# Kernel optimization log

Hardware: AMD Instinct MI355X
Metric: run time of the kernel (lower is better)

## Reference

```python
import jax, jax.numpy as jnp
import numpy as np

B, NPROP, NCLS, NPTS, NBQ, NCK = 32, 256, 19, 4096, 64, 64
C, QH, VQ = 256, 768, 8


def setup_inputs() -> dict:
    key = jax.random.key(0)
    ks = jax.random.split(key, 12)
    s = 0.02
    return dict(
        sem_cls_logits=jax.random.normal(ks[0], (B, NPROP, NCLS), jnp.float32),
        prop_features=jax.random.normal(ks[1], (B, NPROP, C), jnp.float32),
        box_corners=jax.random.normal(ks[2], (B, NPROP, 8, 3), jnp.float32),
        enc_xyz=jax.random.uniform(ks[3], (B, NPTS, 3), jnp.float32),
        enc_features=jax.random.normal(ks[4], (B, NPTS, C), jnp.float32),
        pc_min=jnp.zeros((B, 3), jnp.float32),
        pc_max=jnp.ones((B, 3), jnp.float32),
        box_query=jax.random.normal(ks[5], (B, NBQ, 8, 3), jnp.float32),
        box_qmask=jnp.ones((B, NBQ), jnp.float32),
        click_query=jax.random.uniform(ks[6], (B, NCK, 3), jnp.float32),
        click_qmask=jnp.ones((B, NCK), jnp.float32),
        gauss_B=jax.random.normal(ks[7], (3, C // 2), jnp.float32),
        box_w1=jax.random.normal(ks[8], (C, QH), jnp.float32) * s,
        box_b1=jnp.zeros((QH,), jnp.float32),
        box_w2=jax.random.normal(ks[9], (QH, VQ * QH), jnp.float32) * s,
        box_b2=jnp.zeros((VQ * QH,), jnp.float32),
        click_w1=jax.random.normal(ks[10], (2 * C, QH), jnp.float32) * s,
        click_b1=jnp.zeros((QH,), jnp.float32),
        click_w2=jax.random.normal(ks[11], (QH, VQ * QH), jnp.float32) * s,
        click_b2=jnp.zeros((VQ * QH,), jnp.float32),
    )


def _mlp(x, w1, b1, w2, b2):
    h = jax.nn.relu(jnp.einsum('bqc,ch->bqh', x, w1) + b1)
    return jnp.einsum('bqh,ho->bqo', h, w2) + b2


def _forward(sem_cls_logits, prop_features, box_corners, enc_xyz, enc_features,
             pc_min, pc_max, box_query, box_qmask, click_query, click_qmask,
             gauss_B, box_w1, box_b1, box_w2, box_b2,
             click_w1, click_b1, click_w2, click_b2):
    bsz = sem_cls_logits.shape[0]
    # proposal semantic mask: 0 for background (last class)
    prop_sem_mask = (jnp.argmax(sem_cls_logits, -1) != sem_cls_logits.shape[-1] - 1)
    prop_sem_mask = prop_sem_mask.astype(prop_features.dtype)  # [B, nprop]

    # ---- box branch: axis-aligned 3D IoU from box corners, argmax match, gather ----
    mn_p = box_corners.min(-2)  # [B, nprop, 3]
    mx_p = box_corners.max(-2)
    vol_p = jnp.prod(mx_p - mn_p, -1)  # [B, nprop]
    mn_q = box_query.min(-2)   # [B, nq, 3]
    mx_q = box_query.max(-2)
    vol_q = jnp.prod(mx_q - mn_q, -1)  # [B, nq]
    inter = jnp.prod(
        jnp.clip(jnp.minimum(mx_q[:, :, None], mx_p[:, None]) -
                 jnp.maximum(mn_q[:, :, None], mn_p[:, None]), 0.0, None), -1)  # [B,nq,nprop]
    iou = inter / (vol_q[:, :, None] + vol_p[:, None] - inter + 1e-8)
    iou = iou * prop_sem_mask[:, None, :]
    match_idx = jnp.argmax(iou, -1)  # [B, nq]
    box_feat = jnp.take_along_axis(prop_features, match_idx[..., None], axis=1)  # [B,nq,C]
    box_prompt = _mlp(box_feat, box_w1, box_b1, box_w2, box_b2).reshape(bsz, -1, QH)
    box_mask = jnp.repeat(box_qmask[:, :, None], VQ, axis=2).reshape(bsz, -1)

    # ---- click branch: fourier pos emb + nearest-neighbor gather + MLP ----
    xyz01 = (click_query - pc_min[:, None]) / (pc_max - pc_min)[:, None]
    proj = (xyz01 * (2.0 * jnp.pi)) @ gauss_B  # [B, nclick, C//2]
    pos = jnp.concatenate([jnp.sin(proj), jnp.cos(proj)], -1)  # [B, nclick, C]
    # squared distances (argmin equivalent to cdist argmin)
    d2 = jnp.sum((click_query[:, :, None, :] - enc_xyz[:, None, :, :]) ** 2, -1)  # [B,nclick,npts]
    nn_ids = jnp.argmin(d2, -1)  # [B, nclick]
    k_fea = jnp.take_along_axis(enc_features, nn_ids[..., None], axis=1)  # [B,nclick,C]
    click_in = jnp.concatenate([k_fea, pos], -1)  # [B, nclick, 2C]
    click_prompt = _mlp(click_in, click_w1, click_b1, click_w2, click_b2).reshape(bsz, -1, QH)
    click_mask = jnp.repeat(click_qmask[:, :, None], VQ, axis=2).reshape(bsz, -1)

    prompt_feature = jnp.concatenate([box_prompt, click_prompt], axis=1)  # [B,(nq+nclick)*VQ,QH]
    prompt_mask = jnp.concatenate([box_mask, click_mask], axis=1)
    return prompt_feature, prompt_mask


def reference(sem_cls_logits, prop_features, box_corners, enc_xyz, enc_features,
              pc_min, pc_max, box_query, box_qmask, click_query, click_qmask,
              gauss_B, box_w1, box_b1, box_w2, box_b2,
              click_w1, click_b1, click_w2, click_b2):
    return _forward(sem_cls_logits, prop_features, box_corners, enc_xyz, enc_features,
                    pc_min, pc_max, box_query, box_qmask, click_query, click_qmask,
                    gauss_B, box_w1, box_b1, box_w2, box_b2,
                    click_w1, click_b1, click_w2, click_b2)
```

## Files before the change

kernel.cpp:

```cpp
#include <hip/hip_runtime.h>

#define TWO_PI 6.283185307179586f

typedef _Float16 half8 __attribute__((ext_vector_type(8)));
typedef _Float16 half4 __attribute__((ext_vector_type(4)));
typedef float floatx4 __attribute__((ext_vector_type(4)));

__device__ __forceinline__ void async16(const _Float16* g, _Float16* l) {
    __builtin_amdgcn_global_load_lds(
        (const __attribute__((address_space(1))) void*)g,
        (__attribute__((address_space(3))) void*)l, 16, 0, 0);
}

__global__ void prep_prop(const float* __restrict__ logits,
                          const float* __restrict__ corners,
                          float* __restrict__ mn, float* __restrict__ mx,
                          float* __restrict__ vol, float* __restrict__ msk)
{
    int idx = blockIdx.x * 256 + threadIdx.x;
    const float* c = corners + (size_t)idx * 24;
    float mn0 = c[0], mn1 = c[1], mn2 = c[2];
    float mx0 = mn0, mx1 = mn1, mx2 = mn2;
#pragma unroll
    for (int k = 1; k < 8; k++) {
        float v0 = c[k*3+0], v1 = c[k*3+1], v2 = c[k*3+2];
        mn0 = fminf(mn0, v0); mx0 = fmaxf(mx0, v0);
        mn1 = fminf(mn1, v1); mx1 = fmaxf(mx1, v1);
        mn2 = fminf(mn2, v2); mx2 = fmaxf(mx2, v2);
    }
    mn[idx*3+0] = mn0; mn[idx*3+1] = mn1; mn[idx*3+2] = mn2;
    mx[idx*3+0] = mx0; mx[idx*3+1] = mx1; mx[idx*3+2] = mx2;
    vol[idx] = (mx0-mn0)*(mx1-mn1)*(mx2-mn2);
    const float* lg = logits + (size_t)idx * 19;
    float bv = lg[0]; int bi = 0;
#pragma unroll
    for (int k = 1; k < 19; k++) { float v = lg[k]; if (v > bv) { bv = v; bi = k; } }
    msk[idx] = (bi != 18) ? 1.0f : 0.0f;
}

__global__ void box_match(const float* __restrict__ box_query,
                          const float* __restrict__ mn_p, const float* __restrict__ mx_p,
                          const float* __restrict__ vol_p, const float* __restrict__ msk,
                          int* __restrict__ match_idx)
{
    int gq = blockIdx.x * 256 + threadIdx.x;
    int b = gq >> 6;
    const float* cq = box_query + (size_t)gq * 24;
    float mn0 = cq[0], mn1 = cq[1], mn2 = cq[2];
    float mx0 = mn0, mx1 = mn1, mx2 = mn2;
#pragma unroll
    for (int k = 1; k < 8; k++) {
        float v0 = cq[k*3+0], v1 = cq[k*3+1], v2 = cq[k*3+2];
        mn0 = fminf(mn0, v0); mx0 = fmaxf(mx0, v0);
        mn1 = fminf(mn1, v1); mx1 = fmaxf(mx1, v1);
        mn2 = fminf(mn2, v2); mx2 = fmaxf(mx2, v2);
    }
    float volq = (mx0-mn0)*(mx1-mn1)*(mx2-mn2);
    const float* mnb = mn_p + (size_t)b * 768;
    const float* mxb = mx_p + (size_t)b * 768;
    const float* vb  = vol_p + (size_t)b * 256;
    const float* mb  = msk + (size_t)b * 256;
    float best = -1.0f; int bi = 0;
    for (int p = 0; p < 256; p++) {
        float e0 = fminf(mx0, mxb[p*3+0]) - fmaxf(mn0, mnb[p*3+0]); e0 = fmaxf(e0, 0.0f);
        float e1 = fminf(mx1, mxb[p*3+1]) - fmaxf(mn1, mnb[p*3+1]); e1 = fmaxf(e1, 0.0f);
        float e2 = fminf(mx2, mxb[p*3+2]) - fmaxf(mn2, mnb[p*3+2]); e2 = fmaxf(e2, 0.0f);
        float inter = (e0*e1)*e2;
        float iou = inter / (volq + vb[p] - inter + 1e-8f) * mb[p];
        if (iou > best) { best = iou; bi = p; }
    }
    match_idx[gq] = bi;
}

__global__ void click_nn(const float* __restrict__ click_query,
                         const float* __restrict__ enc_xyz,
                         int* __restrict__ nn_ids)
{
    int gq = blockIdx.x * 4 + (threadIdx.x >> 6);
    int lane = threadIdx.x & 63;
    int b = gq >> 6;
    float cx = click_query[gq*3+0];
    float cy = click_query[gq*3+1];
    float cz = click_query[gq*3+2];
    const float* ex = enc_xyz + (size_t)b * 4096 * 3;
    float best = 3.4e38f; int bidx = 0;
    for (int p = lane; p < 4096; p += 64) {
        float dx = cx - ex[p*3+0];
        float dy = cy - ex[p*3+1];
        float dz = cz - ex[p*3+2];
        float d = dx*dx + dy*dy;
        d = d + dz*dz;
        if (d < best) { best = d; bidx = p; }
    }
#pragma unroll
    for (int off = 32; off; off >>= 1) {
        float ov = __shfl_down(best, off);
        int   oi = __shfl_down(bidx, off);
        if (ov < best || (ov == best && oi < bidx)) { best = ov; bidx = oi; }
    }
    if (lane == 0) nn_ids[gq] = bidx;
}

__global__ void gather_pos(const float* __restrict__ prop_features,
                           const float* __restrict__ enc_features,
                           const int* __restrict__ match_idx,
                           const int* __restrict__ nn_ids,
                           const float* __restrict__ cq,
                           const float* __restrict__ pc_min,
                           const float* __restrict__ pc_max,
                           const float* __restrict__ gB,
                           _Float16* __restrict__ box_in,
                           _Float16* __restrict__ click_in)
{
    int row = blockIdx.x;
    int c = threadIdx.x;
    int b = row >> 6;
    box_in[(size_t)row*256 + c] =
        (_Float16)prop_features[((size_t)b*256 + match_idx[row])*256 + c];
    click_in[(size_t)row*512 + c] =
        (_Float16)enc_features[((size_t)b*4096 + nn_ids[row])*256 + c];
    int j = c & 127;
    float m0 = pc_min[b*3+0], m1 = pc_min[b*3+1], m2 = pc_min[b*3+2];
    float tx = (cq[row*3+0] - m0) / (pc_max[b*3+0] - m0) * TWO_PI;
    float ty = (cq[row*3+1] - m1) / (pc_max[b*3+1] - m1) * TWO_PI;
    float tz = (cq[row*3+2] - m2) / (pc_max[b*3+2] - m2) * TWO_PI;
    float p = tx * gB[j] + ty * gB[128+j] + tz * gB[256+j];
    float v = (c < 128) ? sinf(p) : cosf(p);
    click_in[(size_t)row*512 + 256 + c] = (_Float16)v;
}

__device__ __forceinline__ void transpose_core(
    const float* __restrict__ src, _Float16* __restrict__ dst,
    int K, int N, _Float16* t)
{
    int n0 = blockIdx.x * 64, k0 = blockIdx.y * 64;
    int tid = threadIdx.x;
    int r = tid >> 4;
    int c4 = (tid & 15) * 4;
#pragma unroll
    for (int p = 0; p < 4; p++) {
        int k = r + p*16;
        float4 v = *(const float4*)(src + (size_t)(k0+k)*N + n0 + c4);
        t[(c4+0)*68 + k] = (_Float16)v.x;
        t[(c4+1)*68 + k] = (_Float16)v.y;
        t[(c4+2)*68 + k] = (_Float16)v.z;
        t[(c4+3)*68 + k] = (_Float16)v.w;
    }
    __syncthreads();
    int ck = (tid & 15) * 4;
#pragma unroll
    for (int p = 0; p < 4; p++) {
        int n = r + p*16;
        half4 v = *(const half4*)(t + n*68 + ck);
        *(half4*)(dst + (size_t)(n0+n)*K + k0 + ck) = v;
    }
}

__global__ void transpose_w2(const float* __restrict__ s0, const float* __restrict__ s1,
                             _Float16* __restrict__ d0, _Float16* __restrict__ d1)
{
    __shared__ _Float16 t[64*68];
    if (blockIdx.z == 0) transpose_core(s0, d0, 768, 6144, t);
    else                 transpose_core(s1, d1, 768, 6144, t);
}

__global__ void transpose_w1(const float* __restrict__ s0, const float* __restrict__ s1,
                             _Float16* __restrict__ d0, _Float16* __restrict__ d1)
{
    __shared__ _Float16 t[64*68];
    if (blockIdx.z == 0) {
        if (blockIdx.y * 64 >= 256) return;
        transpose_core(s0, d0, 256, 768, t);
    } else {
        transpose_core(s1, d1, 512, 768, t);
    }
}

template<int MODE>
__device__ __forceinline__ void gemm_core(
    const _Float16* __restrict__ A, const _Float16* __restrict__ Bt,
    const float* __restrict__ bias, int N, int K,
    _Float16* __restrict__ Hout, float* __restrict__ Fout, long brOff,
    _Float16* As, _Float16* Bs)
{
    const int tid = threadIdx.x;
    const int wave = tid >> 6, lane = tid & 63;
    const int bm = blockIdx.x, bn = blockIdx.y;
    const int waveM = (wave & 1) * 64, waveN = (wave >> 1) * 64;
    const int sr = tid >> 2;
    const int sk = (tid & 3) * 8;
    const int nrow = lane & 15, kgrp = (lane >> 4) * 8;

    floatx4 acc[4][4];
#pragma unroll
    for (int i = 0; i < 4; i++)
#pragma unroll
        for (int j = 0; j < 4; j++) { floatx4 z = {0.f,0.f,0.f,0.f}; acc[i][j] = z; }

    const _Float16* Ar0 = A  + (size_t)(bm*128 + sr) * K + sk;
    const _Float16* Ar1 = Ar0 + (size_t)64 * K;
    const _Float16* Br0 = Bt + (size_t)(bn*128 + sr) * K + sk;
    const _Float16* Br1 = Br0 + (size_t)64 * K;
    _Float16* lA0 = As + wave*512;
    _Float16* lA1 = As + 2048 + wave*512;
    _Float16* lB0 = Bs + wave*512;
    _Float16* lB1 = Bs + 2048 + wave*512;

    for (int kk = 0; kk < K; kk += 32) {
        __syncthreads();
        async16(Ar0 + kk, lA0);
        async16(Ar1 + kk, lA1);
        async16(Br0 + kk, lB0);
        async16(Br1 + kk, lB1);
        __syncthreads();
        half8 af[4], bf[4];
#pragma unroll
        for (int i = 0; i < 4; i++)
            af[i] = *(const half8*)(As + (waveM + i*16 + nrow)*32 + kgrp);
#pragma unroll
        for (int j = 0; j < 4; j++)
            bf[j] = *(const half8*)(Bs + (waveN + j*16 + nrow)*32 + kgrp);
#pragma unroll
        for (int i = 0; i < 4; i++)
#pragma unroll
            for (int j = 0; j < 4; j++)
                acc[i][j] = __builtin_amdgcn_mfma_f32_16x16x32_f16(af[i], bf[j], acc[i][j], 0, 0, 0);
    }

#pragma unroll
    for (int i = 0; i < 4; i++) {
#pragma unroll
        for (int j = 0; j < 4; j++) {
            int col = bn*128 + waveN + j*16 + nrow;
            float bv = bias[col];
#pragma unroll
            for (int r = 0; r < 4; r++) {
                int row = bm*128 + waveM + i*16 + (lane >> 4)*4 + r;
                float v = acc[i][j][r] + bv;
                if (MODE == 0) {
                    v = v > 0.f ? v : 0.f;
                    Hout[(size_t)row * N + col] = (_Float16)v;
                } else {
                    size_t off = (size_t)(row >> 6) * 786432 + (size_t)brOff
                               + (size_t)(row & 63) * 6144 + col;
                    Fout[off] = v;
                }
            }
        }
    }
}

__global__ __launch_bounds__(256) void gemm_l1(
    const _Float16* __restrict__ A0, const _Float16* __restrict__ A1,
    const _Float16* __restrict__ B0, const _Float16* __restrict__ B1,
    const float* __restrict__ b0, const float* __restrict__ b1,
    _Float16* __restrict__ H0, _Float16* __restrict__ H1)
{
    __shared__ _Float16 As[4096];
    __shared__ _Float16 Bs[4096];
    if (blockIdx.z == 0)
        gemm_core<0>(A0, B0, b0, 768, 256, H0, nullptr, 0, As, Bs);
    else
        gemm_core<0>(A1, B1, b1, 768, 512, H1, nullptr, 0, As, Bs);
}

__global__ __launch_bounds__(256) void gemm_l2(
    const _Float16* __restrict__ A0, const _Float16* __restrict__ A1,
    const _Float16* __restrict__ B0, const _Float16* __restrict__ B1,
    const float* __restrict__ b0, const float* __restrict__ b1,
    float* __restrict__ out)
{
    __shared__ _Float16 As[4096];
    __shared__ _Float16 Bs[4096];
    if (blockIdx.z == 0)
        gemm_core<1>(A0, B0, b0, 6144, 768, nullptr, out, 0, As, Bs);
    else
        gemm_core<1>(A1, B1, b1, 6144, 768, nullptr, out, 393216, As, Bs);
}

__global__ void write_mask(const float* __restrict__ box_qmask,
                           const float* __restrict__ click_qmask,
                           float* __restrict__ out)
{
    int idx = blockIdx.x * 256 + threadIdx.x;
    int b = idx >> 10, i = idx & 1023;
    float v = (i < 512) ? box_qmask[b*64 + (i >> 3)]
                        : click_qmask[b*64 + ((i - 512) >> 3)];
    out[25165824 + idx] = v;
}

extern "C" void kernel_launch(void* const* d_in, const int* in_sizes, int n_in,
                              void* d_out, int out_size, void* d_ws, size_t ws_size,
                              hipStream_t stream)
{
    const float* sem   = (const float*)d_in[0];
    const float* propf = (const float*)d_in[1];
    const float* boxc  = (const float*)d_in[2];
    const float* encx  = (const float*)d_in[3];
    const float* encf  = (const float*)d_in[4];
    const float* pcmin = (const float*)d_in[5];
    const float* pcmax = (const float*)d_in[6];
    const float* boxq  = (const float*)d_in[7];
    const float* boxm  = (const float*)d_in[8];
    const float* clkq  = (const float*)d_in[9];
    const float* clkm  = (const float*)d_in[10];
    const float* gB    = (const float*)d_in[11];
    const float* bw1   = (const float*)d_in[12];
    const float* bb1   = (const float*)d_in[13];
    const float* bw2   = (const float*)d_in[14];
    const float* bb2   = (const float*)d_in[15];
    const float* cw1   = (const float*)d_in[16];
    const float* cb1   = (const float*)d_in[17];
    const float* cw2   = (const float*)d_in[18];
    const float* cb2   = (const float*)d_in[19];
    float* out = (float*)d_out;
    char* ws = (char*)d_ws;

    float* p_mn  = (float*)(ws + 0);
    float* p_mx  = (float*)(ws + 98304);
    float* p_vol = (float*)(ws + 196608);
    float* p_msk = (float*)(ws + 229376);
    int* midx    = (int*)(ws + 262144);
    int* nnids   = (int*)(ws + 270336);
    _Float16* box_in   = (_Float16*)(ws + 278528);
    _Float16* click_in = (_Float16*)(ws + 1327104);
    _Float16* h_box    = (_Float16*)(ws + 3424256);
    _Float16* h_click  = (_Float16*)(ws + 6569984);
    _Float16* w1t_box  = (_Float16*)(ws + 9715712);
    _Float16* w2t_box  = (_Float16*)(ws + 10108928);
    _Float16* w1t_clk  = (_Float16*)(ws + 19546112);
    _Float16* w2t_clk  = (_Float16*)(ws + 20332544);

    prep_prop<<<32, 256, 0, stream>>>(sem, boxc, p_mn, p_mx, p_vol, p_msk);
    box_match<<<8, 256, 0, stream>>>(boxq, p_mn, p_mx, p_vol, p_msk, midx);
    click_nn<<<512, 256, 0, stream>>>(clkq, encx, nnids);
    gather_pos<<<2048, 256, 0, stream>>>(propf, encf, midx, nnids,
                                         clkq, pcmin, pcmax, gB, box_in, click_in);

    transpose_w1<<<dim3(12, 8, 2),  256, 0, stream>>>(bw1, cw1, w1t_box, w1t_clk);
    transpose_w2<<<dim3(96, 12, 2), 256, 0, stream>>>(bw2, cw2, w2t_box, w2t_clk);

    gemm_l1<<<dim3(16, 6, 2),  256, 0, stream>>>(box_in, click_in, w1t_box, w1t_clk,
                                                 bb1, cb1, h_box, h_click);
    gemm_l2<<<dim3(16, 48, 2), 256, 0, stream>>>(h_box, h_click, w2t_box, w2t_clk,
                                                 bb2, cb2, out);

    write_mask<<<128, 256, 0, stream>>>(boxm, clkm, out);
}
```

Measured before the change: 391.4 us.

## Fuse box prep/match kernels, fold mask write, deepen GEMM K-tile with swizzled LDS

Merges the proposal preprocessing and the box IoU matching into one per-batch kernel that keeps proposal boxes in shared memory, and folds the mask write into the gather kernel, removing two launches. The GEMM core now loads a K-tile of 64 instead of 32 per stage, using an XOR-swizzled LDS layout to avoid bank conflicts, which halves the number of barrier pairs. LDS per block doubles, which may lower occupancy.

```diff
diff --git a/kernel.cpp b/kernel.cpp
--- a/kernel.cpp
+++ b/kernel.cpp
@@ -12,64 +12,58 @@
         (__attribute__((address_space(3))) void*)l, 16, 0, 0);
 }
 
-__global__ void prep_prop(const float* __restrict__ logits,
-                          const float* __restrict__ corners,
-                          float* __restrict__ mn, float* __restrict__ mx,
-                          float* __restrict__ vol, float* __restrict__ msk)
-{
-    int idx = blockIdx.x * 256 + threadIdx.x;
-    const float* c = corners + (size_t)idx * 24;
-    float mn0 = c[0], mn1 = c[1], mn2 = c[2];
-    float mx0 = mn0, mx1 = mn1, mx2 = mn2;
-#pragma unroll
-    for (int k = 1; k < 8; k++) {
-        float v0 = c[k*3+0], v1 = c[k*3+1], v2 = c[k*3+2];
-        mn0 = fminf(mn0, v0); mx0 = fmaxf(mx0, v0);
-        mn1 = fminf(mn1, v1); mx1 = fmaxf(mx1, v1);
-        mn2 = fminf(mn2, v2); mx2 = fmaxf(mx2, v2);
-    }
-    mn[idx*3+0] = mn0; mn[idx*3+1] = mn1; mn[idx*3+2] = mn2;
-    mx[idx*3+0] = mx0; mx[idx*3+1] = mx1; mx[idx*3+2] = mx2;
-    vol[idx] = (mx0-mn0)*(mx1-mn1)*(mx2-mn2);
-    const float* lg = logits + (size_t)idx * 19;
-    float bv = lg[0]; int bi = 0;
-#pragma unroll
-    for (int k = 1; k < 19; k++) { float v = lg[k]; if (v > bv) { bv = v; bi = k; } }
-    msk[idx] = (bi != 18) ? 1.0f : 0.0f;
-}
-
-__global__ void box_match(const float* __restrict__ box_query,
-                          const float* __restrict__ mn_p, const float* __restrict__ mx_p,
-                          const float* __restrict__ vol_p, const float* __restrict__ msk,
-                          int* __restrict__ match_idx)
-{
-    int gq = blockIdx.x * 256 + threadIdx.x;
-    int b = gq >> 6;
-    const float* cq = box_query + (size_t)gq * 24;
-    float mn0 = cq[0], mn1 = cq[1], mn2 = cq[2];
-    float mx0 = mn0, mx1 = mn1, mx2 = mn2;
-#pragma unroll
-    for (int k = 1; k < 8; k++) {
-        float v0 = cq[k*3+0], v1 = cq[k*3+1], v2 = cq[k*3+2];
-        mn0 = fminf(mn0, v0); mx0 = fmaxf(mx0, v0);
-        mn1 = fminf(mn1, v1); mx1 = fmaxf(mx1, v1);
-        mn2 = fminf(mn2, v2); mx2 = fmaxf(mx2, v2);
-    }
-    float volq = (mx0-mn0)*(mx1-mn1)*(mx2-mn2);
-    const float* mnb = mn_p + (size_t)b * 768;
-    const float* mxb = mx_p + (size_t)b * 768;
-    const float* vb  = vol_p + (size_t)b * 256;
-    const float* mb  = msk + (size_t)b * 256;
-    float best = -1.0f; int bi = 0;
-    for (int p = 0; p < 256; p++) {
-        float e0 = fminf(mx0, mxb[p*3+0]) - fmaxf(mn0, mnb[p*3+0]); e0 = fmaxf(e0, 0.0f);
-        float e1 = fminf(mx1, mxb[p*3+1]) - fmaxf(mn1, mnb[p*3+1]); e1 = fmaxf(e1, 0.0f);
-        float e2 = fminf(mx2, mxb[p*3+2]) - fmaxf(mn2, mnb[p*3+2]); e2 = fmaxf(e2, 0.0f);
-        float inter = (e0*e1)*e2;
-        float iou = inter / (volq + vb[p] - inter + 1e-8f) * mb[p];
-        if (iou > best) { best = iou; bi = p; }
-    }
-    match_idx[gq] = bi;
+__global__ void prep_box(const float* __restrict__ logits,
+                         const float* __restrict__ corners,
+                         const float* __restrict__ box_query,
+                         int* __restrict__ match_idx)
+{
+    __shared__ float smn[256][3], smx[256][3], svol[256], smsk[256];
+    int b = blockIdx.x, t = threadIdx.x;
+    {
+        const float* c = corners + ((size_t)b*256 + t) * 24;
+        float mn0 = c[0], mn1 = c[1], mn2 = c[2];
+        float mx0 = mn0, mx1 = mn1, mx2 = mn2;
+#pragma unroll
+        for (int k = 1; k < 8; k++) {
+            float v0 = c[k*3+0], v1 = c[k*3+1], v2 = c[k*3+2];
+            mn0 = fminf(mn0, v0); mx0 = fmaxf(mx0, v0);
+            mn1 = fminf(mn1, v1); mx1 = fmaxf(mx1, v1);
+            mn2 = fminf(mn2, v2); mx2 = fmaxf(mx2, v2);
+        }
+        smn[t][0] = mn0; smn[t][1] = mn1; smn[t][2] = mn2;
+        smx[t][0] = mx0; smx[t][1] = mx1; smx[t][2] = mx2;
+        svol[t] = (mx0-mn0)*(mx1-mn1)*(mx2-mn2);
+        const float* lg = logits + ((size_t)b*256 + t) * 19;
+        float bv = lg[0]; int bi = 0;
+#pragma unroll
+        for (int k = 1; k < 19; k++) { float v = lg[k]; if (v > bv) { bv = v; bi = k; } }
+        smsk[t] = (bi != 18) ? 1.0f : 0.0f;
+    }
+    __syncthreads();
+    if (t < 64) {
+        int gq = b*64 + t;
+        const float* cq = box_query + (size_t)gq * 24;
+        float mn0 = cq[0], mn1 = cq[1], mn2 = cq[2];
+        float mx0 = mn0, mx1 = mn1, mx2 = mn2;
+#pragma unroll
+        for (int k = 1; k < 8; k++) {
+            float v0 = cq[k*3+0], v1 = cq[k*3+1], v2 = cq[k*3+2];
+            mn0 = fminf(mn0, v0); mx0 = fmaxf(mx0, v0);
+            mn1 = fminf(mn1, v1); mx1 = fmaxf(mx1, v1);
+            mn2 = fminf(mn2, v2); mx2 = fmaxf(mx2, v2);
+        }
+        float volq = (mx0-mn0)*(mx1-mn1)*(mx2-mn2);
+        float best = -1.0f; int bi = 0;
+        for (int p = 0; p < 256; p++) {
+            float e0 = fminf(mx0, smx[p][0]) - fmaxf(mn0, smn[p][0]); e0 = fmaxf(e0, 0.0f);
+            float e1 = fminf(mx1, smx[p][1]) - fmaxf(mn1, smn[p][1]); e1 = fmaxf(e1, 0.0f);
+            float e2 = fminf(mx2, smx[p][2]) - fmaxf(mn2, smn[p][2]); e2 = fmaxf(e2, 0.0f);
+            float inter = (e0*e1)*e2;
+            float iou = inter / (volq + svol[p] - inter + 1e-8f) * smsk[p];
+            if (iou > best) { best = iou; bi = p; }
+        }
+        match_idx[gq] = bi;
+    }
 }
 
 __global__ void click_nn(const float* __restrict__ click_query,
@@ -109,8 +103,11 @@
                            const float* __restrict__ pc_min,
                            const float* __restrict__ pc_max,
                            const float* __restrict__ gB,
+                           const float* __restrict__ box_qmask,
+                           const float* __restrict__ click_qmask,
                            _Float16* __restrict__ box_in,
-                           _Float16* __restrict__ click_in)
+                           _Float16* __restrict__ click_in,
+                           float* __restrict__ out)
 {
     int row = blockIdx.x;
     int c = threadIdx.x;
@@ -127,6 +124,13 @@
     float p = tx * gB[j] + ty * gB[128+j] + tz * gB[256+j];
     float v = (c < 128) ? sinf(p) : cosf(p);
     click_in[(size_t)row*512 + 256 + c] = (_Float16)v;
+    if (c < 16) {
+        int idx = row*16 + c;
+        int mb = idx >> 10, i = idx & 1023;
+        float mv = (i < 512) ? box_qmask[mb*64 + (i >> 3)]
+                             : click_qmask[mb*64 + ((i - 512) >> 3)];
+        out[25165824 + idx] = mv;
+    }
 }
 
 __device__ __forceinline__ void transpose_core(
@@ -187,9 +191,11 @@
     const int wave = tid >> 6, lane = tid & 63;
     const int bm = blockIdx.x, bn = blockIdx.y;
     const int waveM = (wave & 1) * 64, waveN = (wave >> 1) * 64;
-    const int sr = tid >> 2;
-    const int sk = (tid & 3) * 8;
-    const int nrow = lane & 15, kgrp = (lane >> 4) * 8;
+    const int nrow = lane & 15;
+    const int kq   = lane >> 4;
+
+    const int srow = tid >> 3;
+    const int jdat = ((tid & 7) ^ (srow & 7)) * 8;
 
     floatx4 acc[4][4];
 #pragma unroll
@@ -197,34 +203,39 @@
 #pragma unroll
         for (int j = 0; j < 4; j++) { floatx4 z = {0.f,0.f,0.f,0.f}; acc[i][j] = z; }
 
-    const _Float16* Ar0 = A  + (size_t)(bm*128 + sr) * K + sk;
-    const _Float16* Ar1 = Ar0 + (size_t)64 * K;
-    const _Float16* Br0 = Bt + (size_t)(bn*128 + sr) * K + sk;
-    const _Float16* Br1 = Br0 + (size_t)64 * K;
-    _Float16* lA0 = As + wave*512;
-    _Float16* lA1 = As + 2048 + wave*512;
-    _Float16* lB0 = Bs + wave*512;
-    _Float16* lB1 = Bs + 2048 + wave*512;
-
-    for (int kk = 0; kk < K; kk += 32) {
+    const _Float16* Ab[4]; const _Float16* Bb[4];
+    _Float16 *lA[4], *lB[4];
+#pragma unroll
+    for (int q = 0; q < 4; q++) {
+        Ab[q] = A  + (size_t)(bm*128 + q*32 + srow) * K + jdat;
+        Bb[q] = Bt + (size_t)(bn*128 + q*32 + srow) * K + jdat;
+        lA[q] = As + q*2048 + wave*512;
+        lB[q] = Bs + q*2048 + wave*512;
+    }
+
+    for (int kk = 0; kk < K; kk += 64) {
         __syncthreads();
-        async16(Ar0 + kk, lA0);
-        async16(Ar1 + kk, lA1);
-        async16(Br0 + kk, lB0);
-        async16(Br1 + kk, lB1);
+#pragma unroll
+        for (int q = 0; q < 4; q++) async16(Ab[q] + kk, lA[q]);
+#pragma unroll
+        for (int q = 0; q < 4; q++) async16(Bb[q] + kk, lB[q]);
         __syncthreads();
-        half8 af[4], bf[4];
-#pragma unroll
-        for (int i = 0; i < 4; i++)
-            af[i] = *(const half8*)(As + (waveM + i*16 + nrow)*32 + kgrp);
-#pragma unroll
-        for (int j = 0; j < 4; j++)
-            bf[j] = *(const half8*)(Bs + (waveN + j*16 + nrow)*32 + kgrp);
-#pragma unroll
-        for (int i = 0; i < 4; i++)
+#pragma unroll
+        for (int h = 0; h < 2; h++) {
+            const int sw = (((kq + h*4) ^ (nrow & 7)) * 8);
+            half8 af[4], bf[4];
+#pragma unroll
+            for (int i = 0; i < 4; i++)
+                af[i] = *(const half8*)(As + (waveM + i*16 + nrow)*64 + sw);
 #pragma unroll
             for (int j = 0; j < 4; j++)
-                acc[i][j] = __builtin_amdgcn_mfma_f32_16x16x32_f16(af[i], bf[j], acc[i][j], 0, 0, 0);
+                bf[j] = *(const half8*)(Bs + (waveN + j*16 + nrow)*64 + sw);
+#pragma unroll
+            for (int i = 0; i < 4; i++)
+#pragma unroll
+                for (int j = 0; j < 4; j++)
+                    acc[i][j] = __builtin_amdgcn_mfma_f32_16x16x32_f16(af[i], bf[j], acc[i][j], 0, 0, 0);
+        }
     }
 
 #pragma unroll
@@ -235,7 +246,7 @@
             float bv = bias[col];
 #pragma unroll
             for (int r = 0; r < 4; r++) {
-                int row = bm*128 + waveM + i*16 + (lane >> 4)*4 + r;
+                int row = bm*128 + waveM + i*16 + kq*4 + r;
                 float v = acc[i][j][r] + bv;
                 if (MODE == 0) {
                     v = v > 0.f ? v : 0.f;
@@ -256,8 +267,8 @@
     const float* __restrict__ b0, const float* __restrict__ b1,
     _Float16* __restrict__ H0, _Float16* __restrict__ H1)
 {
-    __shared__ _Float16 As[4096];
-    __shared__ _Float16 Bs[4096];
+    __shared__ _Float16 As[8192];
+    __shared__ _Float16 Bs[8192];
     if (blockIdx.z == 0)
         gemm_core<0>(A0, B0, b0, 768, 256, H0, nullptr, 0, As, Bs);
     else
@@ -270,23 +281,12 @@
     const float* __restrict__ b0, const float* __restrict__ b1,
     float* __restrict__ out)
 {
-    __shared__ _Float16 As[4096];
-    __shared__ _Float16 Bs[4096];
+    __shared__ _Float16 As[8192];
+    __shared__ _Float16 Bs[8192];
     if (blockIdx.z == 0)
         gemm_core<1>(A0, B0, b0, 6144, 768, nullptr, out, 0, As, Bs);
     else
         gemm_core<1>(A1, B1, b1, 6144, 768, nullptr, out, 393216, As, Bs);
-}
-
-__global__ void write_mask(const float* __restrict__ box_qmask,
-                           const float* __restrict__ click_qmask,
-                           float* __restrict__ out)
-{
-    int idx = blockIdx.x * 256 + threadIdx.x;
-    int b = idx >> 10, i = idx & 1023;
-    float v = (i < 512) ? box_qmask[b*64 + (i >> 3)]
-                        : click_qmask[b*64 + ((i - 512) >> 3)];
-    out[25165824 + idx] = v;
 }
 
 extern "C" void kernel_launch(void* const* d_in, const int* in_sizes, int n_in,
@@ -316,10 +316,6 @@
     float* out = (float*)d_out;
     char* ws = (char*)d_ws;
 
-    float* p_mn  = (float*)(ws + 0);
-    float* p_mx  = (float*)(ws + 98304);
-    float* p_vol = (float*)(ws + 196608);
-    float* p_msk = (float*)(ws + 229376);
     int* midx    = (int*)(ws + 262144);
     int* nnids   = (int*)(ws + 270336);
     _Float16* box_in   = (_Float16*)(ws + 278528);
@@ -331,11 +327,11 @@
     _Float16* w1t_clk  = (_Float16*)(ws + 19546112);
     _Float16* w2t_clk  = (_Float16*)(ws + 20332544);
 
-    prep_prop<<<32, 256, 0, stream>>>(sem, boxc, p_mn, p_mx, p_vol, p_msk);
-    box_match<<<8, 256, 0, stream>>>(boxq, p_mn, p_mx, p_vol, p_msk, midx);
+    prep_box<<<32, 256, 0, stream>>>(sem, boxc, boxq, midx);
     click_nn<<<512, 256, 0, stream>>>(clkq, encx, nnids);
     gather_pos<<<2048, 256, 0, stream>>>(propf, encf, midx, nnids,
-                                         clkq, pcmin, pcmax, gB, box_in, click_in);
+                                         clkq, pcmin, pcmax, gB,
+                                         boxm, clkm, box_in, click_in, out);
 
     transpose_w1<<<dim3(12, 8, 2),  256, 0, stream>>>(bw1, cw1, w1t_box, w1t_clk);
     transpose_w2<<<dim3(96, 12, 2), 256, 0, stream>>>(bw2, cw2, w2t_box, w2t_clk);
@@ -344,6 +340,4 @@
                                                  bb1, cb1, h_box, h_click);
     gemm_l2<<<dim3(16, 48, 2), 256, 0, stream>>>(h_box, h_click, w2t_box, w2t_clk,
                                                  bb2, cb2, out);
-
-    write_mask<<<128, 256, 0, stream>>>(boxm, clkm, out);
-}
+}
```

Result: faster. 372.1 us (-4.9%).
